# Optimization experiments

Hardware: AMD Instinct MI355X
Metric: run time of the kernel (lower is better)

## Reference

```python
import jax, jax.numpy as jnp
import numpy as np

# Single-qubit physics:
#   |0> --RY(theta)--> Bloch z = cos(theta); RZ(phi) leaves z unchanged.
#   AmplitudeDamping(gamma): z' = gamma + (1 - gamma) * z
#   Chained over n_steps: z_N = cos(theta) * P + (1 - P), with P = prod_k (1 - gamma_k)
#   expval(PauliZ) = z_N.  This is the exact closed form of the qml circuit.

B = 16_777_216  # batch of samples
N_STEPS = 64


def setup_inputs() -> dict:
    key = jax.random.key(0)
    k1, k2, k3 = jax.random.split(key, 3)
    thetas = jax.random.normal(k1, (B,), dtype=jnp.float32)
    phis = jax.random.normal(k2, (B,), dtype=jnp.float32)
    raw_gammas = jax.random.normal(k3, (N_STEPS,), dtype=jnp.float32)
    return {"thetas": thetas, "phis": phis, "raw_gammas": raw_gammas}


def reference(thetas, phis, raw_gammas):
    gammas = jax.nn.sigmoid(raw_gammas)                  # [n_steps]
    surv = jnp.prod(1.0 - gammas)                        # scalar P = prod(1-gamma)
    # phis only rotate about Z and do not affect <Z>; kept for faithfulness.
    expvals = jnp.cos(thetas) * surv + (1.0 - surv)      # [B]
    return expvals, gammas
```

## Files before the change

kernel.cpp:

```cpp
#include <hip/hip_runtime.h>

#define B_TOTAL 16777216
#define NSTEPS 64

__global__ void qm_gamma_kernel(const float* __restrict__ raw_gammas,
                                float* __restrict__ out_gammas,
                                float* __restrict__ surv_out) {
    const int lane = threadIdx.x;
    float rg = raw_gammas[lane];
    float g = 1.0f / (1.0f + expf(-rg));
    out_gammas[lane] = g;
    float v = 1.0f - g;
    #pragma unroll
    for (int off = 32; off > 0; off >>= 1) {
        v *= __shfl_xor(v, off, 64);
    }
    if (lane == 0) {
        surv_out[0] = v;
    }
}

__global__ void qm_expval_kernel(const float* __restrict__ thetas,
                                 const float* __restrict__ surv_ptr,
                                 float* __restrict__ out) {
    const float surv = surv_ptr[0];
    const float oms = 1.0f - surv;

    const float4* __restrict__ t4 = reinterpret_cast<const float4*>(thetas);
    float4* __restrict__ o4 = reinterpret_cast<float4*>(out);
    const int n4 = B_TOTAL / 4;

    int idx = blockIdx.x * blockDim.x + threadIdx.x;
    const int stride = gridDim.x * blockDim.x;

    for (int i = idx; i < n4; i += stride) {
        float4 t = t4[i];
        float4 r;
        r.x = fmaf(cosf(t.x), surv, oms);
        r.y = fmaf(cosf(t.y), surv, oms);
        r.z = fmaf(cosf(t.z), surv, oms);
        r.w = fmaf(cosf(t.w), surv, oms);
        o4[i] = r;
    }
}

extern "C" void kernel_launch(void* const* d_in, const int* in_sizes, int n_in,
                              void* d_out, int out_size, void* d_ws, size_t ws_size,
                              hipStream_t stream) {
    const float* thetas = (const float*)d_in[0];
    const float* raw_gammas = (const float*)d_in[2];

    float* out_expvals = (float*)d_out;
    float* out_gammas = (float*)d_out + B_TOTAL;
    float* surv = (float*)d_ws;

    qm_gamma_kernel<<<1, 64, 0, stream>>>(raw_gammas, out_gammas, surv);

    const int block = 256;
    const int grid = 2048;
    qm_expval_kernel<<<grid, block, 0, stream>>>(thetas, surv, out_expvals);
}
```

Measured before the change: 30.66 us.

## Fuse gamma reduction into expval kernel and use fast cosine intrinsics

Merges the single-wave sigmoid/product kernel into the main elementwise kernel. Each block recomputes the survival product from the 64 raw gammas and passes it through shared memory, and block 0 writes the gammas output. This removes one launch and the dependency through global memory. It also switches cosf/expf to the __cosf/__expf fast intrinsics and unrolls the grid-stride loop, trading accuracy for fewer ALU instructions, which may exceed tolerance for large theta arguments.

Result: faster. 26.99 us (-12.0%).

```diff
diff --git a/kernel.cpp b/kernel.cpp
--- a/kernel.cpp
+++ b/kernel.cpp
@@ -3,43 +3,47 @@
 #define B_TOTAL 16777216
 #define NSTEPS 64
 
-__global__ void qm_gamma_kernel(const float* __restrict__ raw_gammas,
-                                float* __restrict__ out_gammas,
-                                float* __restrict__ surv_out) {
-    const int lane = threadIdx.x;
-    float rg = raw_gammas[lane];
-    float g = 1.0f / (1.0f + expf(-rg));
-    out_gammas[lane] = g;
-    float v = 1.0f - g;
-    #pragma unroll
-    for (int off = 32; off > 0; off >>= 1) {
-        v *= __shfl_xor(v, off, 64);
+__global__ void __launch_bounds__(256) qm_fused_kernel(
+        const float* __restrict__ thetas,
+        const float* __restrict__ raw_gammas,
+        float* __restrict__ out_expvals,
+        float* __restrict__ out_gammas) {
+    __shared__ float s_surv;
+    const int tid = threadIdx.x;
+
+    if (tid < 64) {
+        float rg = raw_gammas[tid];
+        float g = 1.0f / (1.0f + __expf(-rg));
+        if (blockIdx.x == 0) {
+            out_gammas[tid] = g;
+        }
+        float v = 1.0f - g;
+        #pragma unroll
+        for (int off = 32; off > 0; off >>= 1) {
+            v *= __shfl_xor(v, off, 64);
+        }
+        if (tid == 0) s_surv = v;
     }
-    if (lane == 0) {
-        surv_out[0] = v;
-    }
-}
+    __syncthreads();
 
-__global__ void qm_expval_kernel(const float* __restrict__ thetas,
-                                 const float* __restrict__ surv_ptr,
-                                 float* __restrict__ out) {
-    const float surv = surv_ptr[0];
+    const float surv = s_surv;
     const float oms = 1.0f - surv;
 
     const float4* __restrict__ t4 = reinterpret_cast<const float4*>(thetas);
-    float4* __restrict__ o4 = reinterpret_cast<float4*>(out);
+    float4* __restrict__ o4 = reinterpret_cast<float4*>(out_expvals);
     const int n4 = B_TOTAL / 4;
 
     int idx = blockIdx.x * blockDim.x + threadIdx.x;
     const int stride = gridDim.x * blockDim.x;
 
+    #pragma unroll 4
     for (int i = idx; i < n4; i += stride) {
         float4 t = t4[i];
         float4 r;
-        r.x = fmaf(cosf(t.x), surv, oms);
-        r.y = fmaf(cosf(t.y), surv, oms);
-        r.z = fmaf(cosf(t.z), surv, oms);
-        r.w = fmaf(cosf(t.w), surv, oms);
+        r.x = fmaf(__cosf(t.x), surv, oms);
+        r.y = fmaf(__cosf(t.y), surv, oms);
+        r.z = fmaf(__cosf(t.z), surv, oms);
+        r.w = fmaf(__cosf(t.w), surv, oms);
         o4[i] = r;
     }
 }
@@ -52,11 +56,9 @@
 
     float* out_expvals = (float*)d_out;
     float* out_gammas = (float*)d_out + B_TOTAL;
-    float* surv = (float*)d_ws;
-
-    qm_gamma_kernel<<<1, 64, 0, stream>>>(raw_gammas, out_gammas, surv);
 
     const int block = 256;
     const int grid = 2048;
-    qm_expval_kernel<<<grid, block, 0, stream>>>(thetas, surv, out_expvals);
+    qm_fused_kernel<<<grid, block, 0, stream>>>(thetas, raw_gammas,
+                                                out_expvals, out_gammas);
 }
```
